# Performance work log

Hardware: AMD Instinct MI355X
Metric: run time of the kernel (lower is better)

The kernel has to match this reference:

```python
import jax, jax.numpy as jnp
import numpy as np

N_NODES = 25000
N_EDGES = 500000
ND, ED, G = 32, 19, 200


def _lrelu(x):
    return jax.nn.leaky_relu(x, 0.01)


def setup_inputs() -> dict:
    key = jax.random.key(0)
    ks = jax.random.split(key, 12)
    s = 0.05
    return {
        "node_feats": jax.random.normal(ks[0], (N_NODES, ND), jnp.float32),
        "edge_feats": jax.random.normal(ks[1], (N_EDGES, ED), jnp.float32),
        "src": jax.random.randint(ks[2], (N_EDGES,), 0, N_NODES),
        "dst": jax.random.randint(ks[3], (N_EDGES,), 0, N_NODES),
        "Wn": jax.random.normal(ks[4], (G, ND), jnp.float32) * s,
        "bn": jnp.zeros((G,), jnp.float32),
        "We1": jax.random.normal(ks[5], (G, ND + ED), jnp.float32) * s,
        "be1": jnp.zeros((G,), jnp.float32),
        "We2": jax.random.normal(ks[6], (1, 2 * G), jnp.float32) * s,
        "be2": jnp.zeros((1,), jnp.float32),
        "Wet": jax.random.normal(ks[7], (G, G), jnp.float32) * s,
        "bet": jnp.zeros((G,), jnp.float32),
        "W_ih": jax.random.normal(ks[8], (3 * G, G), jnp.float32) * s,
        "b_ih": jnp.zeros((3 * G,), jnp.float32),
        "W_hh": jax.random.normal(ks[9], (3 * G, G), jnp.float32) * s,
        "b_hh": jnp.zeros((3 * G,), jnp.float32),
    }


def reference(node_feats, edge_feats, src, dst, Wn, bn, We1, be1, We2, be2,
              Wet, bet, W_ih, b_ih, W_hh, b_hh):
    N = node_feats.shape[0]
    # project_node: Linear + LeakyReLU -> hv_new [N, G]
    hv_new = _lrelu(node_feats @ Wn.T + bn)
    # apply_edges1 + project_edge1: cat([src hv, he]) -> he1 [E, G]
    he1 = _lrelu(jnp.concatenate([node_feats[src], edge_feats], axis=1) @ We1.T + be1)
    # apply_edges2 + project_edge2: cat([dst hv_new, he1]) -> logits [E, 1]
    he2 = jnp.concatenate([hv_new[dst], he1], axis=1)
    logits = _lrelu(he2 @ We2.T + be2)[:, 0]  # [E]
    # edge_softmax: softmax over incoming edges per destination node
    m = jax.ops.segment_max(logits, dst, num_segments=N)  # [N]
    ex = jnp.exp(logits - m[dst])
    denom = jax.ops.segment_sum(ex, dst, num_segments=N)  # [N]
    a = ex / denom[dst]  # [E]
    # AttentiveGRU1: e = a * edge_transform(he1); scatter-sum to dst
    e = a[:, None] * (he1 @ Wet.T + bet)  # [E, G]
    c = jax.ops.segment_sum(e, dst, num_segments=N)  # [N, G]
    context = jax.nn.elu(c)
    # GRUCell(context, hv_new)
    gi = context @ W_ih.T + b_ih
    gh = hv_new @ W_hh.T + b_hh
    ir, iz, inn = jnp.split(gi, 3, axis=1)
    hr, hz, hn = jnp.split(gh, 3, axis=1)
    r = jax.nn.sigmoid(ir + hr)
    z = jax.nn.sigmoid(iz + hz)
    n = jnp.tanh(inn + r * hn)
    h = (1.0 - z) * n + z * hv_new
    return jax.nn.relu(h)
```

## Files before the change

kernel.cpp:

```cpp
#include <hip/hip_runtime.h>
#include <hip/hip_bf16.h>

#define G 200
#define NDIM 32
#define EDIM 19
#define KIN 51

typedef unsigned short u16;
typedef unsigned int u32;
typedef unsigned long long u64;

typedef __attribute__((ext_vector_type(8))) short bfrag;
typedef __attribute__((ext_vector_type(4))) float ffrag;

__device__ __forceinline__ float lrelu(float x){ return x > 0.f ? x : 0.01f*x; }
__device__ __forceinline__ u16 f2b(float x){ u32 u = __float_as_uint(x); return (u16)((u + 0x7fffu + ((u >> 16) & 1u)) >> 16); }
__device__ __forceinline__ float b2f(u16 x){ return __uint_as_float(((u32)x) << 16); }
__device__ __forceinline__ u32 f2b2(float a, float b){
  u32 r;
  asm("v_cvt_pk_bf16_f32 %0, %1, %2" : "=v"(r) : "v"(a), "v"(b));
  return r;
}

#define MFMA16(a, b, c) __builtin_amdgcn_mfma_f32_16x16x32_bf16(a, b, c, 0, 0, 0)

__global__ void init_kernel(float* __restrict__ s_raw, float* __restrict__ denom,
                            int* __restrict__ deg, float* __restrict__ l1,
                            const float* __restrict__ nf, u16* __restrict__ nfb,
                            const float* __restrict__ We1, const float* __restrict__ Wn,
                            const float* __restrict__ Wet, const float* __restrict__ Wih,
                            const float* __restrict__ Whh,
                            const float* __restrict__ be1, const float* __restrict__ We2,
                            u16* __restrict__ Wbg, u16* __restrict__ Wnb, u16* __restrict__ Wet2,
                            u16* __restrict__ Wrz, u16* __restrict__ Winn, u16* __restrict__ Whn,
                            u32* __restrict__ bwt, int N){
  int i = blockIdx.x * 256 + threadIdx.x;
  if (i < N * G) s_raw[i] = 0.f;
  if (i < N){ denom[i] = 0.f; deg[i] = 0; l1[i] = 0.f; }
  if (i < N * NDIM) nfb[i] = f2b(nf[i]);
  if (i < 208){
    float bv = (i < G) ? be1[i] : 0.f;
    float wv = (i < G) ? We2[G + i] : 0.f;
    bwt[i] = (u32)f2b(bv) | ((u32)f2b(wv) << 16);
  }

  int idx = i;
  const int s0 = 208 * 64, s1 = 256 * 64, s2 = 208 * 224, s3 = 2 * 208 * 416, s4 = 208 * 224, s5 = 208 * 224;
  if (idx < s0){
    int r = idx >> 6, k = idx & 63;
    Wbg[idx] = f2b((r < G && k < KIN) ? We1[r * KIN + k] : 0.f);
    return;
  }
  idx -= s0;
  if (idx < s1){
    int r = idx >> 6, k = idx & 63;
    Wnb[idx] = f2b((r < G && k < NDIM) ? Wn[r * NDIM + k] : 0.f);
    return;
  }
  idx -= s1;
  if (idx < s2){
    int r = idx / 224, k = idx % 224;
    Wet2[idx] = f2b((r < G && k < G) ? Wet[r * G + k] : 0.f);
    return;
  }
  idx -= s2;
  if (idx < s3){
    int g = idx / (208 * 416), rem = idx % (208 * 416);
    int r = rem / 416, k = rem % 416;
    float v = 0.f;
    if (r < G){
      int row = g * G + r;
      if (k < G) v = Wih[row * G + k];
      else if (k >= 208 && k < 408) v = Whh[row * G + (k - 208)];
    }
    Wrz[idx] = f2b(v);
    return;
  }
  idx -= s3;
  if (idx < s4){
    int r = idx / 224, k = idx % 224;
    Winn[idx] = f2b((r < G && k < G) ? Wih[(2 * G + r) * G + k] : 0.f);
    return;
  }
  idx -= s4;
  if (idx < s5){
    int r = idx / 224, kk = idx % 224;
    Whn[idx] = f2b((r < G && kk >= 16 && kk < 216) ? Whh[(2 * G + r) * G + (kk - 16)] : 0.f);
  }
}

__global__ void deghist_kernel(const int* __restrict__ dst, int* __restrict__ deg, int E){
  int e = blockIdx.x * 256 + threadIdx.x;
  if (e < E) atomicAdd(&deg[dst[e]], 1);
}

__global__ __launch_bounds__(1024) void scan_kernel(const int* __restrict__ deg, int* __restrict__ offs,
                                                    int* __restrict__ cur, int N){
  __shared__ int sd[12800];
  __shared__ int wsums[16];
  const int C = 25;
  int tid = threadIdx.x;
  int lane = tid & 63, wid = tid >> 6;
  int val[C];
  for (int h = 0; h < 2; ++h){
    int base_h = h * 12800;
    for (int k = tid; k < 12800; k += 1024){
      int gi = base_h + k;
      sd[k] = (gi < N) ? deg[gi] : 0;
    }
    __syncthreads();
    if ((tid >> 9) == h){
      int t0 = (tid - h * 512) * C;
      #pragma unroll
      for (int i = 0; i < C; ++i) val[i] = sd[t0 + i];
    }
    __syncthreads();
  }
  int s = 0;
  #pragma unroll
  for (int i = 0; i < C; ++i){ int v = val[i]; val[i] = s; s += v; }
  int x = s;
  #pragma unroll
  for (int off = 1; off < 64; off <<= 1){
    int y = __shfl_up(x, off, 64);
    if (lane >= off) x += y;
  }
  if (lane == 63) wsums[wid] = x;
  __syncthreads();
  if (wid == 0){
    int w = (lane < 16) ? wsums[lane] : 0;
    #pragma unroll
    for (int off = 1; off < 16; off <<= 1){
      int y = __shfl_up(w, off, 64);
      if (lane >= off) w += y;
    }
    if (lane < 16) wsums[lane] = w;
  }
  __syncthreads();
  int excl = ((wid ? wsums[wid - 1] : 0) + x) - s;
  int base = tid * C;
  #pragma unroll
  for (int i = 0; i < C; ++i){
    int o = excl + val[i];
    if (base + i < N){ offs[base + i] = o; cur[base + i] = o; }
  }
  if (tid == 1023) offs[N] = excl + s;
}

__global__ void scatter_pack_kernel(const int* __restrict__ dst, const int* __restrict__ src,
                                    const float* __restrict__ ef, const float* __restrict__ l1,
                                    int* __restrict__ cur, u32* __restrict__ erec, int E){
  int e = blockIdx.x * 256 + threadIdx.x;
  if (e >= E) return;
  int d = dst[e];
  int pos = atomicAdd(&cur[d], 1);
  u32 w[16];
  w[0] = (u32)d; w[1] = (u32)src[e]; w[2] = __float_as_uint(l1[d]); w[3] = 0u;
  const float* ep = ef + (long)e * EDIM;
  #pragma unroll
  for (int j = 0; j < 9; ++j) w[4 + j] = (u32)f2b(ep[2 * j]) | ((u32)f2b(ep[2 * j + 1]) << 16);
  w[13] = (u32)f2b(ep[18]);
  w[14] = 0u; w[15] = 0u;
  uint4* dp = (uint4*)(erec + (size_t)pos * 16);
  dp[0] = make_uint4(w[0], w[1], w[2], w[3]);
  dp[1] = make_uint4(w[4], w[5], w[6], w[7]);
  dp[2] = make_uint4(w[8], w[9], w[10], w[11]);
  dp[3] = make_uint4(w[12], w[13], w[14], w[15]);
}

__global__ __launch_bounds__(256) void hvgemm_kernel(
    const float* __restrict__ nf, const u16* __restrict__ Wnb, const float* __restrict__ bn,
    const float* __restrict__ We2, u16* __restrict__ hvb, float* __restrict__ l1, int M)
{
  __shared__ __align__(16) u16 As[64][72];
  __shared__ __align__(16) u16 Ws[64][72];
  int tid = threadIdx.x;
  int m0 = blockIdx.y * 64, n0 = blockIdx.x * 64;
  int l = tid & 63, w = tid >> 6, quad = l >> 4, col = l & 15;

  for (int idx = tid; idx < 64 * 16; idx += 256){
    int r = idx >> 4, c4 = idx & 15;
    int row = m0 + r, k = c4 * 4;
    float4 v = make_float4(0.f,0.f,0.f,0.f);
    if (row < M && k < NDIM) v = *(const float4*)(nf + (long)row * NDIM + k);
    *(ushort4*)&As[r][c4 * 4] = make_ushort4(f2b(v.x), f2b(v.y), f2b(v.z), f2b(v.w));
  }
  for (int idx = tid; idx < 64 * 8; idx += 256){
    int r = idx >> 3, c = idx & 7;
    *(ulonglong2*)&Ws[r][c * 8] = *(const ulonglong2*)(Wnb + (long)(n0 + r) * 64 + c * 8);
  }
  __syncthreads();
  bfrag a0 = *(const bfrag*)&As[w * 16 + col][quad * 8];
  bfrag a1 = *(const bfrag*)&As[w * 16 + col][32 + quad * 8];
  ffrag acc[4];
  #pragma unroll
  for (int t = 0; t < 4; ++t){ acc[t].x = 0.f; acc[t].y = 0.f; acc[t].z = 0.f; acc[t].w = 0.f; }
  #pragma unroll
  for (int t = 0; t < 4; ++t){
    bfrag b0 = *(const bfrag*)&Ws[t * 16 + col][quad * 8];
    bfrag b1 = *(const bfrag*)&Ws[t * 16 + col][32 + quad * 8];
    acc[t] = MFMA16(a0, b0, acc[t]);
    acc[t] = MFMA16(a1, b1, acc[t]);
  }
  float lp[4] = {0.f, 0.f, 0.f, 0.f};
  #pragma unroll
  for (int t = 0; t < 4; ++t){
    int n = n0 + t * 16 + col;
    float bv = (n < G) ? bn[n] : 0.f;
    float wv = (n < G) ? We2[n] : 0.f;
    #pragma unroll
    for (int r = 0; r < 4; ++r){
      int row = m0 + w * 16 + quad * 4 + r;
      float v = lrelu(acc[t][r] + bv);
      lp[r] += wv * v;
      if (n < G && row < M) hvb[(long)row * G + n] = f2b(v);
    }
  }
  #pragma unroll
  for (int r = 0; r < 4; ++r){
    lp[r] += __shfl_xor(lp[r], 1, 16);
    lp[r] += __shfl_xor(lp[r], 2, 16);
    lp[r] += __shfl_xor(lp[r], 4, 16);
    lp[r] += __shfl_xor(lp[r], 8, 16);
  }
  if (col == 0){
    #pragma unroll
    for (int r = 0; r < 4; ++r){
      int row = m0 + w * 16 + quad * 4 + r;
      if (row < M) atomicAdd(&l1[row], lp[r]);
    }
  }
}

#define SST 72
__global__ __launch_bounds__(128, 2) void edge_csr_kernel(
    const u16* __restrict__ nfb, const u32* __restrict__ erec, const int* __restrict__ offs,
    const u16* __restrict__ Wbg, const u32* __restrict__ bwt, const float* __restrict__ be2,
    float* __restrict__ s_raw, float* __restrict__ denom, int E)
{
  __shared__ __align__(16) u16 shm[208 * SST];
  __shared__ int segnode[64];
  __shared__ __align__(16) u16 exb[64];
  __shared__ __align__(8) unsigned char segb[64];
  __shared__ int Svar;

  int tid = threadIdx.x;
  int j0 = blockIdx.x * 64;
  int l = tid & 63, w = tid >> 6;
  int quad = l >> 4, col = l & 15;
  int m0a = w * 32, m0b = w * 32 + 16;

  int ja = j0 + m0a + col;
  int jb = j0 + m0b + col;
  bool va = ja < E, vb = jb < E;
  int sa = va ? (int)erec[(size_t)ja * 16 + 1] : 0;
  int sb = vb ? (int)erec[(size_t)jb * 16 + 1] : 0;
  bfrag a0a = {0,0,0,0,0,0,0,0}, a1a = {0,0,0,0,0,0,0,0};
  bfrag a0b = {0,0,0,0,0,0,0,0}, a1b = {0,0,0,0,0,0,0,0};
  if (va){
    a0a = *(const bfrag*)(nfb + (long)sa * NDIM + quad * 8);
    if (quad < 3) a1a = *(const bfrag*)((const u16*)erec + (size_t)ja * 32 + 8 + quad * 8);
  }
  if (vb){
    a0b = *(const bfrag*)(nfb + (long)sb * NDIM + quad * 8);
    if (quad < 3) a1b = *(const bfrag*)((const u16*)erec + (size_t)jb * 32 + 8 + quad * 8);
  }

  bfrag B0[13], B1[13];
  u32 bwp[13];
  #pragma unroll
  for (int t = 0; t < 13; ++t){
    B0[t] = *(const bfrag*)(Wbg + (t * 16 + col) * 64 + quad * 8);
    B1[t] = *(const bfrag*)(Wbg + (t * 16 + col) * 64 + 32 + quad * 8);
    bwp[t] = bwt[t * 16 + col];
  }

  if (tid < 64){
    int j = j0 + tid;
    int valid = j < E;
    int n = valid ? (int)erec[(size_t)j * 16] : -1;
    int nn = (tid == 63 || j + 1 >= E) ? -2 : (int)erec[(size_t)(j + 1) * 16];
    int f1 = (valid && n != nn) ? 1 : 0;
    int f2 = 0;
    if (f1 && offs[n] >= j0 && offs[n + 1] <= j0 + 64) f2 = 1;
    u64 em = __ballot(f1 != 0);
    int seg = (int)__popcll(em & ((1ull << tid) - 1ull));
    segb[tid] = (unsigned char)seg;
    if (f1) segnode[seg] = (n << 1) | f2;
    if (tid == 0) Svar = (int)__popcll(em);
    shm[200 * SST + tid] = 0x3F80;
  }

  float pla[4] = {0.f, 0.f, 0.f, 0.f};
  float plb[4] = {0.f, 0.f, 0.f, 0.f};
  #pragma unroll
  for (int t = 0; t < 13; ++t){
    ffrag acca; acca.x = 0.f; acca.y = 0.f; acca.z = 0.f; acca.w = 0.f;
    ffrag accb; accb.x = 0.f; accb.y = 0.f; accb.z = 0.f; accb.w = 0.f;
    acca = MFMA16(a0a, B0[t], acca);
    acca = MFMA16(a1a, B1[t], acca);
    accb = MFMA16(a0b, B0[t], accb);
    accb = MFMA16(a1b, B1[t], accb);
    int g = t * 16 + col;
    u32 bw = bwp[t];
    float bv = b2f((u16)(bw & 0xFFFF)), wv = b2f((u16)(bw >> 16));
    float u0 = lrelu(acca.x + bv), u1 = lrelu(acca.y + bv);
    float u2 = lrelu(acca.z + bv), u3 = lrelu(acca.w + bv);
    pla[0] += wv * u0; pla[1] += wv * u1; pla[2] += wv * u2; pla[3] += wv * u3;
    float v0 = lrelu(accb.x + bv), v1 = lrelu(accb.y + bv);
    float v2 = lrelu(accb.z + bv), v3 = lrelu(accb.w + bv);
    plb[0] += wv * v0; plb[1] += wv * v1; plb[2] += wv * v2; plb[3] += wv * v3;
    if (g < G){
      *(uint2*)&shm[g * SST + m0a + quad * 4] = make_uint2(f2b2(u0, u1), f2b2(u2, u3));
      *(uint2*)&shm[g * SST + m0b + quad * 4] = make_uint2(f2b2(v0, v1), f2b2(v2, v3));
    }
  }
  #pragma unroll
  for (int r = 0; r < 4; ++r){
    pla[r] += __shfl_xor(pla[r], 1, 16);
    pla[r] += __shfl_xor(pla[r], 2, 16);
    pla[r] += __shfl_xor(pla[r], 4, 16);
    pla[r] += __shfl_xor(pla[r], 8, 16);
    plb[r] += __shfl_xor(plb[r], 1, 16);
    plb[r] += __shfl_xor(plb[r], 2, 16);
    plb[r] += __shfl_xor(plb[r], 4, 16);
    plb[r] += __shfl_xor(plb[r], 8, 16);
  }
  if (col == 0){
    #pragma unroll
    for (int r = 0; r < 4; ++r){
      int ea = m0a + quad * 4 + r;
      float exa = 0.f;
      if (j0 + ea < E){
        float l1v = __uint_as_float(erec[(size_t)(j0 + ea) * 16 + 2]);
        exa = __expf(lrelu(pla[r] + l1v + be2[0]));
      }
      exb[ea] = f2b(exa);
      int eb = m0b + quad * 4 + r;
      float exv = 0.f;
      if (j0 + eb < E){
        float l1v = __uint_as_float(erec[(size_t)(j0 + eb) * 16 + 2]);
        exv = __expf(lrelu(plb[r] + l1v + be2[0]));
      }
      exb[eb] = f2b(exv);
    }
  }
  __syncthreads();

  int S = Svar;
  for (int mt = 0; mt * 16 < S; ++mt){
    int m = mt * 16 + col;
    u64 sb0 = *(const u64*)&segb[quad * 8];
    u64 sb1 = *(const u64*)&segb[32 + quad * 8];
    ulonglong2 ew0 = *(const ulonglong2*)&exb[quad * 8];
    ulonglong2 ew1 = *(const ulonglong2*)&exb[32 + quad * 8];
    bfrag A0, A1;
    #pragma unroll
    for (int jj = 0; jj < 8; ++jj){
      int s0i = (int)((sb0 >> (8 * jj)) & 0xFF);
      int s1i = (int)((sb1 >> (8 * jj)) & 0xFF);
      u64 w0 = (jj < 4) ? ew0.x : ew0.y;
      u64 w1 = (jj < 4) ? ew1.x : ew1.y;
      u16 e0 = (u16)(w0 >> (16 * (jj & 3)));
      u16 e1 = (u16)(w1 >> (16 * (jj & 3)));
      A0[jj] = (s0i == m) ? (short)e0 : (short)0;
      A1[jj] = (s1i == m) ? (short)e1 : (short)0;
    }
    int t0 = (w == 0) ? 0 : 7;
    int cnt = (w == 0) ? 7 : 6;
    for (int i = 0; i < cnt; ++i){
      int t = t0 + i;
      bfrag b0 = *(const bfrag*)&shm[(t * 16 + col) * SST + quad * 8];
      bfrag b1 = *(const bfrag*)&shm[(t * 16 + col) * SST + 32 + quad * 8];
      ffrag acc; acc.x = 0.f; acc.y = 0.f; acc.z = 0.f; acc.w = 0.f;
      acc = MFMA16(A0, b0, acc);
      acc = MFMA16(A1, b1, acc);
      int g = t * 16 + col;
      #pragma unroll
      for (int r = 0; r < 4; ++r){
        int seg = mt * 16 + quad * 4 + r;
        if (seg < S && g <= 200){
          int enc = segnode[seg];
          int nd = enc >> 1;
          float v = acc[r];
          float* pd = (g < G) ? (s_raw + (long)nd * G + g) : (denom + nd);
          if (enc & 1) *pd = v; else atomicAdd(pd, v);
        }
      }
    }
  }
}

#define XST 420
__global__ __launch_bounds__(128, 2) void ctxgru_kernel(
    const float* __restrict__ s_raw, const u16* __restrict__ hvb, const float* __restrict__ denom,
    const u16* __restrict__ Wet2, const u16* __restrict__ Wrz,
    const u16* __restrict__ Winn, const u16* __restrict__ Whn,
    const float* __restrict__ bet, const float* __restrict__ b_ih, const float* __restrict__ b_hh,
    float* __restrict__ out, int M)
{
  __shared__ __align__(16) u16 X[32 * XST];
  __shared__ float invds[32];
  int tid = threadIdx.x;
  int m0 = blockIdx.x * 32;

  if (tid < 32){
    float dn = (m0 + tid < M) ? denom[m0 + tid] : 0.f;
    invds[tid] = dn > 0.f ? 1.f / dn : 0.f;
  }
  __syncthreads();

  for (int idx = tid; idx < 32 * 50; idx += 128){
    int r = idx / 50, c = idx % 50;
    int row = m0 + r;
    float4 v = make_float4(0.f,0.f,0.f,0.f);
    ushort4 h = make_ushort4(0,0,0,0);
    if (row < M){
      v = *(const float4*)(s_raw + (long)row * G + c * 4);
      h = *(const ushort4*)(hvb + (long)row * G + c * 4);
    }
    float iv = invds[r];
    *(ushort4*)&X[r * XST + c * 4] = make_ushort4(f2b(v.x*iv), f2b(v.y*iv), f2b(v.z*iv), f2b(v.w*iv));
    *(ushort4*)&X[r * XST + 208 + c * 4] = h;
  }
  for (int idx = tid; idx < 32 * 4; idx += 128){
    int r = idx / 4, q = idx % 4;
    int base = (q < 2) ? (200 + q * 4) : (408 + (q - 2) * 4);
    *(ushort4*)&X[r * XST + base] = make_ushort4(0,0,0,0);
  }
  __syncthreads();

  int l = tid & 63, w = tid >> 6, quad = l >> 4, col = l & 15;
  int rowbase = w * 16;

  bfrag a1[7];
  #pragma unroll
  for (int j = 0; j < 7; ++j) a1[j] = *(const bfrag*)&X[(rowbase + col) * XST + j * 32 + quad * 8];

  for (int st = 0; st < 13; ++st){
    int n = st * 16 + col;
    ffrag acc; acc.x = 0.f; acc.y = 0.f; acc.z = 0.f; acc.w = 0.f;
    #pragma unroll
    for (int j = 0; j < 7; ++j){
      bfrag b = *(const bfrag*)(Wet2 + (long)n * 224 + j * 32 + quad * 8);
      acc = MFMA16(a1[j], b, acc);
    }
    if (n < G){
      float bv = bet[n];
      #pragma unroll
      for (int r = 0; r < 4; ++r){
        int lr = rowbase + quad * 4 + r;
        float gate = invds[lr] > 0.f ? 1.f : 0.f;
        float v = acc[r] + gate * bv;
        v = (v > 0.f) ? v : (__expf(v) - 1.f);
        X[lr * XST + n] = f2b(v);
      }
    }
  }
  __syncthreads();

  bfrag a2[13];
  #pragma unroll
  for (int j = 0; j < 13; ++j) a2[j] = *(const bfrag*)&X[(rowbase + col) * XST + j * 32 + quad * 8];

  for (int st = 0; st < 13; ++st){
    int n = st * 16 + col;
    ffrag ar, az, ai, ah;
    ar.x=ar.y=ar.z=ar.w=0.f; az.x=az.y=az.z=az.w=0.f;
    ai.x=ai.y=ai.z=ai.w=0.f; ah.x=ah.y=ah.z=ah.w=0.f;
    #pragma unroll
    for (int j = 0; j < 13; ++j){
      bfrag br_ = *(const bfrag*)(Wrz + (long)n * 416 + j * 32 + quad * 8);
      ar = MFMA16(a2[j], br_, ar);
      bfrag bz_ = *(const bfrag*)(Wrz + (long)(208 + n) * 416 + j * 32 + quad * 8);
      az = MFMA16(a2[j], bz_, az);
    }
    #pragma unroll
    for (int j = 0; j < 7; ++j){
      bfrag bi_ = *(const bfrag*)(Winn + (long)n * 224 + j * 32 + quad * 8);
      ai = MFMA16(a2[j], bi_, ai);
      bfrag bh_ = *(const bfrag*)(Whn + (long)n * 224 + j * 32 + quad * 8);
      ah = MFMA16(a2[j + 6], bh_, ah);
    }
    if (n < G){
      float br = b_ih[n] + b_hh[n];
      float bz = b_ih[G + n] + b_hh[G + n];
      float bi = b_ih[2 * G + n];
      float bh = b_hh[2 * G + n];
      #pragma unroll
      for (int r = 0; r < 4; ++r){
        int lr = rowbase + quad * 4 + r;
        int row = m0 + lr;
        if (row < M){
          float rg = 1.f / (1.f + __expf(-(ar[r] + br)));
          float zg = 1.f / (1.f + __expf(-(az[r] + bz)));
          float ng = tanhf(ai[r] + bi + rg * (ah[r] + bh));
          float hvv = b2f(X[lr * XST + 208 + n]);
          float h = (1.f - zg) * ng + zg * hvv;
          out[(long)row * G + n] = h > 0.f ? h : 0.f;
        }
      }
    }
  }
}

extern "C" void kernel_launch(void* const* d_in, const int* in_sizes, int n_in,
                              void* d_out, int out_size, void* d_ws, size_t ws_size,
                              hipStream_t stream)
{
  const float* nf   = (const float*)d_in[0];
  const float* ef   = (const float*)d_in[1];
  const int*   src  = (const int*)d_in[2];
  const int*   dst  = (const int*)d_in[3];
  const float* Wn   = (const float*)d_in[4];
  const float* bn   = (const float*)d_in[5];
  const float* We1  = (const float*)d_in[6];
  const float* be1  = (const float*)d_in[7];
  const float* We2  = (const float*)d_in[8];
  const float* be2  = (const float*)d_in[9];
  const float* Wet  = (const float*)d_in[10];
  const float* bet  = (const float*)d_in[11];
  const float* W_ih = (const float*)d_in[12];
  const float* b_ih = (const float*)d_in[13];
  const float* W_hh = (const float*)d_in[14];
  const float* b_hh = (const float*)d_in[15];
  int N = in_sizes[0] / NDIM;
  int E = in_sizes[2];
  float* out = (float*)d_out;

  char* p = (char*)d_ws;
  auto alloc = [&](size_t b){ char* r = p; p += (b + 255) & ~(size_t)255; return r; };
  u16*   hvb   = (u16*)  alloc((size_t)N * G * 2);
  float* s_raw = (float*)alloc((size_t)N * G * 4);
  float* denom = (float*)alloc((size_t)N * 4);
  int*   deg   = (int*)  alloc((size_t)N * 4);
  int*   offs  = (int*)  alloc((size_t)(N + 1) * 4);
  int*   cur   = (int*)  alloc((size_t)N * 4);
  u32*   erec  = (u32*)  alloc((size_t)E * 64);
  u16*   nfb   = (u16*)  alloc((size_t)N * NDIM * 2);
  float* l1    = (float*)alloc((size_t)N * 4);
  u16*   Wbg   = (u16*)  alloc((size_t)208 * 64 * 2);
  u16*   Wnb   = (u16*)  alloc((size_t)256 * 64 * 2);
  u16*   Wet2  = (u16*)  alloc((size_t)208 * 224 * 2);
  u16*   Wrz   = (u16*)  alloc((size_t)2 * 208 * 416 * 2);
  u16*   Winn  = (u16*)  alloc((size_t)208 * 224 * 2);
  u16*   Whn   = (u16*)  alloc((size_t)208 * 224 * 2);
  u32*   bwt   = (u32*)  alloc((size_t)208 * 4);

  int eb = (E + 255) / 256;
  int mb = (N + 63) / 64;
  int mb2 = (N + 31) / 32;

  init_kernel<<<dim3((N * G + 255) / 256), dim3(256), 0, stream>>>(
      s_raw, denom, deg, l1, nf, nfb, We1, Wn, Wet, W_ih, W_hh, be1, We2,
      Wbg, Wnb, Wet2, Wrz, Winn, Whn, bwt, N);
  deghist_kernel<<<dim3(eb), dim3(256), 0, stream>>>(dst, deg, E);
  scan_kernel<<<dim3(1), dim3(1024), 0, stream>>>(deg, offs, cur, N);
  hvgemm_kernel<<<dim3(4, mb), dim3(256), 0, stream>>>(nf, Wnb, bn, We2, hvb, l1, N);
  scatter_pack_kernel<<<dim3(eb), dim3(256), 0, stream>>>(dst, src, ef, l1, cur, erec, E);
  edge_csr_kernel<<<dim3((E + 63) / 64), dim3(128), 0, stream>>>(nfb, erec, offs,
                                                                 Wbg, bwt, be2, s_raw, denom, E);
  ctxgru_kernel<<<dim3(mb2), dim3(128), 0, stream>>>(s_raw, hvb, denom, Wet2, Wrz, Winn, Whn,
                                                     bet, b_ih, b_hh, out, N);
}
```

Before: 408.9 us.

## Use one wave per 32-row block in ctxgru to reuse weight fragments twice

The ctxgru kernel now runs 64 threads per block, and one wave computes both 16-row tiles. Each weight fragment loaded from global memory feeds two MFMAs, which halves the redundant weight traffic per block. The cost is double the accumulator and A-fragment registers (26 A fragments plus 8 accumulators in the GRU stage), which can cause spills or lower occupancy. There are also fewer threads to stage the 32-row tile into shared memory.

```diff
diff --git a/kernel.cpp b/kernel.cpp
--- a/kernel.cpp
+++ b/kernel.cpp
@@ -392,7 +392,7 @@
 }
 
 #define XST 420
-__global__ __launch_bounds__(128, 2) void ctxgru_kernel(
+__global__ __launch_bounds__(64, 2) void ctxgru_kernel(
     const float* __restrict__ s_raw, const u16* __restrict__ hvb, const float* __restrict__ denom,
     const u16* __restrict__ Wet2, const u16* __restrict__ Wrz,
     const u16* __restrict__ Winn, const u16* __restrict__ Whn,
@@ -410,7 +410,7 @@
   }
   __syncthreads();
 
-  for (int idx = tid; idx < 32 * 50; idx += 128){
+  for (int idx = tid; idx < 32 * 50; idx += 64){
     int r = idx / 50, c = idx % 50;
     int row = m0 + r;
     float4 v = make_float4(0.f,0.f,0.f,0.f);
@@ -423,64 +423,81 @@
     *(ushort4*)&X[r * XST + c * 4] = make_ushort4(f2b(v.x*iv), f2b(v.y*iv), f2b(v.z*iv), f2b(v.w*iv));
     *(ushort4*)&X[r * XST + 208 + c * 4] = h;
   }
-  for (int idx = tid; idx < 32 * 4; idx += 128){
+  for (int idx = tid; idx < 32 * 4; idx += 64){
     int r = idx / 4, q = idx % 4;
     int base = (q < 2) ? (200 + q * 4) : (408 + (q - 2) * 4);
     *(ushort4*)&X[r * XST + base] = make_ushort4(0,0,0,0);
   }
   __syncthreads();
 
-  int l = tid & 63, w = tid >> 6, quad = l >> 4, col = l & 15;
-  int rowbase = w * 16;
-
-  bfrag a1[7];
-  #pragma unroll
-  for (int j = 0; j < 7; ++j) a1[j] = *(const bfrag*)&X[(rowbase + col) * XST + j * 32 + quad * 8];
+  int quad = tid >> 4, col = tid & 15;
+
+  bfrag a1a[7], a1b[7];
+  #pragma unroll
+  for (int j = 0; j < 7; ++j){
+    a1a[j] = *(const bfrag*)&X[(col) * XST + j * 32 + quad * 8];
+    a1b[j] = *(const bfrag*)&X[(16 + col) * XST + j * 32 + quad * 8];
+  }
 
   for (int st = 0; st < 13; ++st){
     int n = st * 16 + col;
-    ffrag acc; acc.x = 0.f; acc.y = 0.f; acc.z = 0.f; acc.w = 0.f;
+    ffrag acca; acca.x = 0.f; acca.y = 0.f; acca.z = 0.f; acca.w = 0.f;
+    ffrag accb; accb.x = 0.f; accb.y = 0.f; accb.z = 0.f; accb.w = 0.f;
     #pragma unroll
     for (int j = 0; j < 7; ++j){
       bfrag b = *(const bfrag*)(Wet2 + (long)n * 224 + j * 32 + quad * 8);
-      acc = MFMA16(a1[j], b, acc);
+      acca = MFMA16(a1a[j], b, acca);
+      accb = MFMA16(a1b[j], b, accb);
     }
     if (n < G){
       float bv = bet[n];
       #pragma unroll
       for (int r = 0; r < 4; ++r){
-        int lr = rowbase + quad * 4 + r;
-        float gate = invds[lr] > 0.f ? 1.f : 0.f;
-        float v = acc[r] + gate * bv;
-        v = (v > 0.f) ? v : (__expf(v) - 1.f);
-        X[lr * XST + n] = f2b(v);
+        int lra = quad * 4 + r, lrb = 16 + quad * 4 + r;
+        float ga = invds[lra] > 0.f ? 1.f : 0.f;
+        float gb = invds[lrb] > 0.f ? 1.f : 0.f;
+        float va_ = acca[r] + ga * bv;
+        float vb_ = accb[r] + gb * bv;
+        va_ = (va_ > 0.f) ? va_ : (__expf(va_) - 1.f);
+        vb_ = (vb_ > 0.f) ? vb_ : (__expf(vb_) - 1.f);
+        X[lra * XST + n] = f2b(va_);
+        X[lrb * XST + n] = f2b(vb_);
       }
     }
   }
   __syncthreads();
 
-  bfrag a2[13];
-  #pragma unroll
-  for (int j = 0; j < 13; ++j) a2[j] = *(const bfrag*)&X[(rowbase + col) * XST + j * 32 + quad * 8];
+  bfrag a2a[13], a2b[13];
+  #pragma unroll
+  for (int j = 0; j < 13; ++j){
+    a2a[j] = *(const bfrag*)&X[(col) * XST + j * 32 + quad * 8];
+    a2b[j] = *(const bfrag*)&X[(16 + col) * XST + j * 32 + quad * 8];
+  }
 
   for (int st = 0; st < 13; ++st){
     int n = st * 16 + col;
-    ffrag ar, az, ai, ah;
-    ar.x=ar.y=ar.z=ar.w=0.f; az.x=az.y=az.z=az.w=0.f;
-    ai.x=ai.y=ai.z=ai.w=0.f; ah.x=ah.y=ah.z=ah.w=0.f;
+    ffrag ara, aza, aia, aha, arb, azb, aib, ahb;
+    ara.x=ara.y=ara.z=ara.w=0.f; aza.x=aza.y=aza.z=aza.w=0.f;
+    aia.x=aia.y=aia.z=aia.w=0.f; aha.x=aha.y=aha.z=aha.w=0.f;
+    arb.x=arb.y=arb.z=arb.w=0.f; azb.x=azb.y=azb.z=azb.w=0.f;
+    aib.x=aib.y=aib.z=aib.w=0.f; ahb.x=ahb.y=ahb.z=ahb.w=0.f;
     #pragma unroll
     for (int j = 0; j < 13; ++j){
       bfrag br_ = *(const bfrag*)(Wrz + (long)n * 416 + j * 32 + quad * 8);
-      ar = MFMA16(a2[j], br_, ar);
+      ara = MFMA16(a2a[j], br_, ara);
+      arb = MFMA16(a2b[j], br_, arb);
       bfrag bz_ = *(const bfrag*)(Wrz + (long)(208 + n) * 416 + j * 32 + quad * 8);
-      az = MFMA16(a2[j], bz_, az);
+      aza = MFMA16(a2a[j], bz_, aza);
+      azb = MFMA16(a2b[j], bz_, azb);
     }
     #pragma unroll
     for (int j = 0; j < 7; ++j){
       bfrag bi_ = *(const bfrag*)(Winn + (long)n * 224 + j * 32 + quad * 8);
-      ai = MFMA16(a2[j], bi_, ai);
+      aia = MFMA16(a2a[j], bi_, aia);
+      aib = MFMA16(a2b[j], bi_, aib);
       bfrag bh_ = *(const bfrag*)(Whn + (long)n * 224 + j * 32 + quad * 8);
-      ah = MFMA16(a2[j + 6], bh_, ah);
+      aha = MFMA16(a2a[j + 6], bh_, aha);
+      ahb = MFMA16(a2b[j + 6], bh_, ahb);
     }
     if (n < G){
       float br = b_ih[n] + b_hh[n];
@@ -489,15 +506,25 @@
       float bh = b_hh[2 * G + n];
       #pragma unroll
       for (int r = 0; r < 4; ++r){
-        int lr = rowbase + quad * 4 + r;
-        int row = m0 + lr;
-        if (row < M){
-          float rg = 1.f / (1.f + __expf(-(ar[r] + br)));
-          float zg = 1.f / (1.f + __expf(-(az[r] + bz)));
-          float ng = tanhf(ai[r] + bi + rg * (ah[r] + bh));
-          float hvv = b2f(X[lr * XST + 208 + n]);
+        int lra = quad * 4 + r;
+        int rowa = m0 + lra;
+        if (rowa < M){
+          float rg = 1.f / (1.f + __expf(-(ara[r] + br)));
+          float zg = 1.f / (1.f + __expf(-(aza[r] + bz)));
+          float ng = tanhf(aia[r] + bi + rg * (aha[r] + bh));
+          float hvv = b2f(X[lra * XST + 208 + n]);
           float h = (1.f - zg) * ng + zg * hvv;
-          out[(long)row * G + n] = h > 0.f ? h : 0.f;
+          out[(long)rowa * G + n] = h > 0.f ? h : 0.f;
+        }
+        int lrb = 16 + quad * 4 + r;
+        int rowb = m0 + lrb;
+        if (rowb < M){
+          float rg = 1.f / (1.f + __expf(-(arb[r] + br)));
+          float zg = 1.f / (1.f + __expf(-(azb[r] + bz)));
+          float ng = tanhf(aib[r] + bi + rg * (ahb[r] + bh));
+          float hvv = b2f(X[lrb * XST + 208 + n]);
+          float h = (1.f - zg) * ng + zg * hvv;
+          out[(long)rowb * G + n] = h > 0.f ? h : 0.f;
         }
       }
     }
@@ -560,6 +587,6 @@
   scatter_pack_kernel<<<dim3(eb), dim3(256), 0, stream>>>(dst, src, ef, l1, cur, erec, E);
   edge_csr_kernel<<<dim3((E + 63) / 64), dim3(128), 0, stream>>>(nfb, erec, offs,
                                                                  Wbg, bwt, be2, s_raw, denom, E);
-  ctxgru_kernel<<<dim3(mb2), dim3(128), 0, stream>>>(s_raw, hvb, denom, Wet2, Wrz, Winn, Whn,
-                                                     bet, b_ih, b_hh, out, N);
-}
+  ctxgru_kernel<<<dim3(mb2), dim3(64), 0, stream>>>(s_raw, hvb, denom, Wet2, Wrz, Winn, Whn,
+                                                    bet, b_ih, b_hh, out, N);
+}
```

After: 426.4 us. 1.04x slower.

## Swizzle edge staging LDS and split GRU output columns across waves

Applied to the files above, without the earlier changes.

The edge kernel's shared staging buffer drops its padded stride for a 64-element row with an XOR swizzle on the byte offset, so the bf16 stores and MFMA fragment loads avoid bank conflicts and the buffer shrinks. The ctxgru kernel now takes 16 rows per block instead of 32. Its two waves share those rows and split the 13 output column tiles (7 and 6) between them, where before each wave owned 16 rows. This doubles the block count and cuts LDS per block, but each block reads the weight matrices for only 16 rows, so total weight traffic per node goes up.

```diff
diff --git a/kernel.cpp b/kernel.cpp
--- a/kernel.cpp
+++ b/kernel.cpp
@@ -232,13 +232,19 @@
   }
 }
 
-#define SST 72
+__device__ __forceinline__ u16* stg_ptr(u16* shm, int row, int byte_off){
+  return (u16*)((char*)(shm + row * 64) + (byte_off ^ ((row & 7) << 4)));
+}
+__device__ __forceinline__ const u16* stg_cptr(const u16* shm, int row, int byte_off){
+  return (const u16*)((const char*)(shm + row * 64) + (byte_off ^ ((row & 7) << 4)));
+}
+
 __global__ __launch_bounds__(128, 2) void edge_csr_kernel(
     const u16* __restrict__ nfb, const u32* __restrict__ erec, const int* __restrict__ offs,
     const u16* __restrict__ Wbg, const u32* __restrict__ bwt, const float* __restrict__ be2,
     float* __restrict__ s_raw, float* __restrict__ denom, int E)
 {
-  __shared__ __align__(16) u16 shm[208 * SST];
+  __shared__ __align__(128) u16 shm[208 * 64];
   __shared__ int segnode[64];
   __shared__ __align__(16) u16 exb[64];
   __shared__ __align__(8) unsigned char segb[64];
@@ -288,7 +294,7 @@
     segb[tid] = (unsigned char)seg;
     if (f1) segnode[seg] = (n << 1) | f2;
     if (tid == 0) Svar = (int)__popcll(em);
-    shm[200 * SST + tid] = 0x3F80;
+    *stg_ptr(shm, 200, tid * 2) = 0x3F80;
   }
 
   float pla[4] = {0.f, 0.f, 0.f, 0.f};
@@ -311,8 +317,8 @@
     float v2 = lrelu(accb.z + bv), v3 = lrelu(accb.w + bv);
     plb[0] += wv * v0; plb[1] += wv * v1; plb[2] += wv * v2; plb[3] += wv * v3;
     if (g < G){
-      *(uint2*)&shm[g * SST + m0a + quad * 4] = make_uint2(f2b2(u0, u1), f2b2(u2, u3));
-      *(uint2*)&shm[g * SST + m0b + quad * 4] = make_uint2(f2b2(v0, v1), f2b2(v2, v3));
+      *(uint2*)stg_ptr(shm, g, (m0a + quad * 4) * 2) = make_uint2(f2b2(u0, u1), f2b2(u2, u3));
+      *(uint2*)stg_ptr(shm, g, (m0b + quad * 4) * 2) = make_uint2(f2b2(v0, v1), f2b2(v2, v3));
     }
   }
   #pragma unroll
@@ -370,12 +376,13 @@
     int cnt = (w == 0) ? 7 : 6;
     for (int i = 0; i < cnt; ++i){
       int t = t0 + i;
-      bfrag b0 = *(const bfrag*)&shm[(t * 16 + col) * SST + quad * 8];
-      bfrag b1 = *(const bfrag*)&shm[(t * 16 + col) * SST + 32 + quad * 8];
+      int row = t * 16 + col;
+      bfrag b0 = *(const bfrag*)stg_cptr(shm, row, quad * 16);
+      bfrag b1 = *(const bfrag*)stg_cptr(shm, row, 64 + quad * 16);
       ffrag acc; acc.x = 0.f; acc.y = 0.f; acc.z = 0.f; acc.w = 0.f;
       acc = MFMA16(A0, b0, acc);
       acc = MFMA16(A1, b1, acc);
-      int g = t * 16 + col;
+      int g = row;
       #pragma unroll
       for (int r = 0; r < 4; ++r){
         int seg = mt * 16 + quad * 4 + r;
@@ -399,18 +406,18 @@
     const float* __restrict__ bet, const float* __restrict__ b_ih, const float* __restrict__ b_hh,
     float* __restrict__ out, int M)
 {
-  __shared__ __align__(16) u16 X[32 * XST];
-  __shared__ float invds[32];
+  __shared__ __align__(16) u16 X[16 * XST];
+  __shared__ float invds[16];
   int tid = threadIdx.x;
-  int m0 = blockIdx.x * 32;
-
-  if (tid < 32){
+  int m0 = blockIdx.x * 16;
+
+  if (tid < 16){
     float dn = (m0 + tid < M) ? denom[m0 + tid] : 0.f;
     invds[tid] = dn > 0.f ? 1.f / dn : 0.f;
   }
   __syncthreads();
 
-  for (int idx = tid; idx < 32 * 50; idx += 128){
+  for (int idx = tid; idx < 16 * 50; idx += 128){
     int r = idx / 50, c = idx % 50;
     int row = m0 + r;
     float4 v = make_float4(0.f,0.f,0.f,0.f);
@@ -423,7 +430,7 @@
     *(ushort4*)&X[r * XST + c * 4] = make_ushort4(f2b(v.x*iv), f2b(v.y*iv), f2b(v.z*iv), f2b(v.w*iv));
     *(ushort4*)&X[r * XST + 208 + c * 4] = h;
   }
-  for (int idx = tid; idx < 32 * 4; idx += 128){
+  for (int idx = tid; idx < 16 * 4; idx += 128){
     int r = idx / 4, q = idx % 4;
     int base = (q < 2) ? (200 + q * 4) : (408 + (q - 2) * 4);
     *(ushort4*)&X[r * XST + base] = make_ushort4(0,0,0,0);
@@ -431,13 +438,15 @@
   __syncthreads();
 
   int l = tid & 63, w = tid >> 6, quad = l >> 4, col = l & 15;
-  int rowbase = w * 16;
+  int st0 = (w == 0) ? 0 : 7;
+  int stn = (w == 0) ? 7 : 6;
 
   bfrag a1[7];
   #pragma unroll
-  for (int j = 0; j < 7; ++j) a1[j] = *(const bfrag*)&X[(rowbase + col) * XST + j * 32 + quad * 8];
-
-  for (int st = 0; st < 13; ++st){
+  for (int j = 0; j < 7; ++j) a1[j] = *(const bfrag*)&X[col * XST + j * 32 + quad * 8];
+
+  for (int ii = 0; ii < stn; ++ii){
+    int st = st0 + ii;
     int n = st * 16 + col;
     ffrag acc; acc.x = 0.f; acc.y = 0.f; acc.z = 0.f; acc.w = 0.f;
     #pragma unroll
@@ -449,7 +458,7 @@
       float bv = bet[n];
       #pragma unroll
       for (int r = 0; r < 4; ++r){
-        int lr = rowbase + quad * 4 + r;
+        int lr = quad * 4 + r;
         float gate = invds[lr] > 0.f ? 1.f : 0.f;
         float v = acc[r] + gate * bv;
         v = (v > 0.f) ? v : (__expf(v) - 1.f);
@@ -461,9 +470,10 @@
 
   bfrag a2[13];
   #pragma unroll
-  for (int j = 0; j < 13; ++j) a2[j] = *(const bfrag*)&X[(rowbase + col) * XST + j * 32 + quad * 8];
-
-  for (int st = 0; st < 13; ++st){
+  for (int j = 0; j < 13; ++j) a2[j] = *(const bfrag*)&X[col * XST + j * 32 + quad * 8];
+
+  for (int ii = 0; ii < stn; ++ii){
+    int st = st0 + ii;
     int n = st * 16 + col;
     ffrag ar, az, ai, ah;
     ar.x=ar.y=ar.z=ar.w=0.f; az.x=az.y=az.z=az.w=0.f;
@@ -489,7 +499,7 @@
       float bh = b_hh[2 * G + n];
       #pragma unroll
       for (int r = 0; r < 4; ++r){
-        int lr = rowbase + quad * 4 + r;
+        int lr = quad * 4 + r;
         int row = m0 + lr;
         if (row < M){
           float rg = 1.f / (1.f + __expf(-(ar[r] + br)));
@@ -549,7 +559,7 @@
 
   int eb = (E + 255) / 256;
   int mb = (N + 63) / 64;
-  int mb2 = (N + 31) / 32;
+  int mb3 = (N + 15) / 16;
 
   init_kernel<<<dim3((N * G + 255) / 256), dim3(256), 0, stream>>>(
       s_raw, denom, deg, l1, nf, nfb, We1, Wn, Wet, W_ih, W_hh, be1, We2,
@@ -560,6 +570,6 @@
   scatter_pack_kernel<<<dim3(eb), dim3(256), 0, stream>>>(dst, src, ef, l1, cur, erec, E);
   edge_csr_kernel<<<dim3((E + 63) / 64), dim3(128), 0, stream>>>(nfb, erec, offs,
                                                                  Wbg, bwt, be2, s_raw, denom, E);
-  ctxgru_kernel<<<dim3(mb2), dim3(128), 0, stream>>>(s_raw, hvb, denom, Wet2, Wrz, Winn, Whn,
+  ctxgru_kernel<<<dim3(mb3), dim3(128), 0, stream>>>(s_raw, hvb, denom, Wet2, Wrz, Winn, Whn,
                                                      bet, b_ih, b_hh, out, N);
 }
```

After: 412.7 us. Within noise of the previous version (+0.9%).
